# Optimization experiments

Hardware: AMD Instinct MI355X
Metric: run time of the kernel (lower is better)

Reference implementation:

```python
import jax, jax.numpy as jnp
import numpy as np

IN_U = 1024
OUT_U = 1024
BATCH = 4096
HID = 20            # ceil(log2(IN_U*OUT_U)), layer_encoding_dim=0 since num_layers=1
MLP_H = 10
FEAT = 3 + 3 * HID  # 63


def setup_inputs() -> dict:
    key = jax.random.key(0)
    ks = jax.random.split(key, 6)
    X = jax.random.normal(ks[0], (BATCH, IN_U), dtype=jnp.float32)
    weight = jax.random.normal(ks[1], (IN_U, OUT_U), dtype=jnp.float32) * 0.02
    # binary positional encodings per cell (encode_weight_hidden_states)
    k = jnp.arange(IN_U * OUT_U, dtype=jnp.int32).reshape(IN_U, OUT_U)
    shifts = jnp.arange(HID - 1, -1, -1, dtype=jnp.int32)
    hidden = ((k[..., None] >> shifts) & 1).astype(jnp.float32)  # [IN_U, OUT_U, HID]
    W1 = jax.random.normal(ks[2], (FEAT, MLP_H), dtype=jnp.float32) / np.float32(np.sqrt(FEAT))
    b1 = jnp.zeros((MLP_H,), jnp.float32)
    W2 = jax.random.normal(ks[3], (MLP_H, MLP_H), dtype=jnp.float32) / np.float32(np.sqrt(MLP_H))
    b2 = jnp.zeros((MLP_H,), jnp.float32)
    W3 = jax.random.normal(ks[4], (MLP_H, 1 + HID), dtype=jnp.float32) / np.float32(np.sqrt(MLP_H))
    b3 = jnp.zeros((1 + HID,), jnp.float32)
    return {"X": X, "weight": weight, "hidden": hidden,
            "W1": W1, "b1": b1, "W2": W2, "b2": b2, "W3": W3, "b3": b3}


def reference(X, weight, hidden, W1, b1, W2, b2, W3, b3):
    n, m = weight.shape
    # exclude-self column means ('forward') and row means ('backward')
    fwd_mean = (jnp.sum(weight, axis=0, keepdims=True) - weight) / (n - 1)   # [n,m]
    bwd_mean = (jnp.sum(weight, axis=1, keepdims=True) - weight) / (m - 1)   # [n,m]
    fwd_hs = (jnp.sum(hidden, axis=0, keepdims=True) - hidden) / (n - 1)     # [n,m,H]
    bwd_hs = (jnp.sum(hidden, axis=1, keepdims=True) - hidden) / (m - 1)     # [n,m,H]
    feat = jnp.concatenate(
        [weight[..., None], fwd_mean[..., None], bwd_mean[..., None],
         hidden, fwd_hs, bwd_hs], axis=-1)                                   # [n,m,3+3H]
    h = jax.nn.relu(jnp.einsum('nmf,fh->nmh', feat, W1) + b1)
    h = jax.nn.relu(jnp.einsum('nmh,hk->nmk', h, W2) + b2)
    updates = jnp.einsum('nmk,ko->nmo', h, W3) + b3                          # [n,m,1+H]
    new_weight = weight + updates[..., 0]
    # (hidden states also get updates[...,1:] in the torch module, but only the
    #  softmax output is returned)
    logits = jax.nn.relu(X @ new_weight)                                     # [B,m]
    return jax.nn.softmax(logits, axis=-1)
```

## Files before the change

kernel.cpp:

```cpp
#include <hip/hip_runtime.h>
#include <hip/hip_bf16.h>
#include <stdint.h>


#define RS_OFF      0
#define CSPART_OFF  4096
#define BT_OFF      266240
#define AH_OFF      4460544

typedef __attribute__((ext_vector_type(8))) _Float16 f16x8;
typedef __attribute__((ext_vector_type(4))) float f32x4;

__device__ __forceinline__ unsigned short f2h(float x) {
    _Float16 h = (_Float16)x;
    unsigned short u;
    __builtin_memcpy(&u, &h, 2);
    return u;
}
__device__ __forceinline__ float h2f(unsigned short u) {
    _Float16 h;
    __builtin_memcpy(&h, &u, 2);
    return (float)h;
}
__device__ __forceinline__ void gld16(const void* g, void* l) {
    __builtin_amdgcn_global_load_lds(
        (const __attribute__((address_space(1))) unsigned*)g,
        (__attribute__((address_space(3))) unsigned*)l, 16, 0, 0);
}

__global__ __launch_bounds__(256) void k_pre(const float* __restrict__ w,
        float* __restrict__ rs, float* __restrict__ cs_part) {
    __shared__ float part[4][1024];
    int t = threadIdx.x;
    int lane = t & 63, wv = t >> 6;
    int r0 = blockIdx.x * 16 + wv * 4;
    float ccol[16];
    #pragma unroll
    for (int j = 0; j < 16; ++j) ccol[j] = 0.f;
    #pragma unroll
    for (int rr = 0; rr < 4; ++rr) {
        int row = r0 + rr;
        float rsum = 0.f;
        #pragma unroll
        for (int j = 0; j < 16; ++j) {
            float v = w[(size_t)row * 1024 + j * 64 + lane];
            ccol[j] += v;
            rsum += v;
        }
        #pragma unroll
        for (int o = 32; o; o >>= 1) rsum += __shfl_down(rsum, o);
        if (lane == 0) rs[row] = rsum;
    }
    #pragma unroll
    for (int j = 0; j < 16; ++j) part[wv][j * 64 + lane] = ccol[j];
    __syncthreads();
    #pragma unroll
    for (int j = 0; j < 4; ++j) {
        int c = t + j * 256;
        cs_part[(size_t)blockIdx.x * 1024 + c] =
            part[0][c] + part[1][c] + part[2][c] + part[3][c];
    }
}

__global__ __launch_bounds__(256) void k_nw(const float* __restrict__ w,
        const float* __restrict__ X,
        const float* __restrict__ rs, const float* __restrict__ cs_part,
        const float* __restrict__ W1, const float* __restrict__ b1,
        const float* __restrict__ W2, const float* __restrict__ b2,
        const float* __restrict__ W3, const float* __restrict__ b3,
        unsigned short* __restrict__ Bt, unsigned short* __restrict__ Ah) {
    __shared__ float sW1[630], sW2[100], sb1[10], sb2[10], sw3[10], sa[10];
    __shared__ float rs_loc[32], cs_loc[32];
    __shared__ float rn_loc[320], cm_loc[320];
    __shared__ float st[32][33];
    int t = threadIdx.x;
    if (blockIdx.x >= 1024) {
        int b2x = blockIdx.x - 1024;
        #pragma unroll
        for (int p = 0; p < 4; ++p) {
            size_t idx = (size_t)b2x * 4096 + p * 1024 + t * 4;
            float4 v = *(const float4*)&X[idx];
            ushort4 h;
            h.x = f2h(v.x); h.y = f2h(v.y); h.z = f2h(v.z); h.w = f2h(v.w);
            *(ushort4*)&Ah[idx] = h;
        }
        return;
    }
    int n0 = (blockIdx.x & 31) * 32;
    int m0 = (blockIdx.x >> 5) * 32;
    const float inv = 1.0f / 1023.0f;

    for (int i = t; i < 630; i += 256) sW1[i] = W1[i];
    if (t < 100) sW2[t] = W2[t];
    if (t >= 128 && t < 138) { sb1[t - 128] = b1[t - 128]; sb2[t - 128] = b2[t - 128]; }
    if (t >= 160 && t < 170) sw3[t - 160] = W3[(t - 160) * 21];
    if (t >= 192 && t < 224) rs_loc[t - 192] = rs[n0 + t - 192];
    if (t >= 224 && t < 256) {
        float s = 0.f;
        #pragma unroll
        for (int p = 0; p < 64; ++p) s += cs_part[(size_t)p * 1024 + m0 + (t - 224)];
        cs_loc[t - 224] = s;
    }
    float b30 = b3[0];
    __syncthreads();
    if (t < 10) sa[t] = sW1[t] - (sW1[10 + t] + sW1[20 + t]) * inv;
    for (int id = t; id < 640; id += 256) {
        int h = id % 10, i = (id / 10) & 31, side = id >= 320;
        if (!side) {
            int n = n0 + i;
            float v = rs_loc[i] * sW1[20 + h] * inv;
            #pragma unroll
            for (int j = 0; j < 10; j++) {
                float bit = (float)((n >> (9 - j)) & 1);
                v += bit * (sW1[(3 + j) * 10 + h] + sW1[(43 + j) * 10 + h]
                            - sW1[(23 + j) * 10 + h] * inv);
                v += (512.0f * inv) * sW1[(23 + j) * 10 + h];
            }
            rn_loc[i * 10 + h] = v;
        } else {
            int m = m0 + i;
            float v = cs_loc[i] * sW1[10 + h] * inv + sb1[h];
            #pragma unroll
            for (int j = 0; j < 10; j++) {
                float bit = (float)((m >> (9 - j)) & 1);
                v += bit * (sW1[(13 + j) * 10 + h] + sW1[(33 + j) * 10 + h]
                            - sW1[(53 + j) * 10 + h] * inv);
                v += (512.0f * inv) * sW1[(53 + j) * 10 + h];
            }
            cm_loc[i * 10 + h] = v;
        }
    }
    __syncthreads();
    int ml = t & 31;
    #pragma unroll
    for (int i = 0; i < 4; i++) {
        int nl = (t >> 5) + 8 * i;
        float wv = w[(size_t)(n0 + nl) * 1024 + m0 + ml];
        float h1[10];
        #pragma unroll
        for (int h = 0; h < 10; h++)
            h1[h] = fmaxf(wv * sa[h] + rn_loc[nl * 10 + h] + cm_loc[ml * 10 + h], 0.f);
        float u = b30;
        #pragma unroll
        for (int k = 0; k < 10; k++) {
            float h2 = sb2[k];
            #pragma unroll
            for (int h = 0; h < 10; h++) h2 += h1[h] * sW2[h * 10 + k];
            u += fmaxf(h2, 0.f) * sw3[k];
        }
        st[nl][ml] = wv + u;
    }
    __syncthreads();
    int mrow = t >> 3, kc = t & 7;
    unsigned short hi4[4], lo4[4];
    #pragma unroll
    for (int j = 0; j < 4; j++) {
        float v = st[kc * 4 + j][mrow];
        unsigned short h = f2h(v);
        hi4[j] = h;
        lo4[j] = f2h(v - h2f(h));
    }
    size_t base = (size_t)(m0 + mrow) * 2048 + n0 + kc * 4;
    *(ushort4*)&Bt[base]        = make_ushort4(hi4[0], hi4[1], hi4[2], hi4[3]);
    *(ushort4*)&Bt[base + 1024] = make_ushort4(lo4[0], lo4[1], lo4[2], lo4[3]);
}

__global__ __launch_bounds__(256, 3) void k_gemm6(const unsigned short* __restrict__ Ah,
        const unsigned short* __restrict__ Bt, float* __restrict__ out) {
    __shared__ unsigned short sAh[128 * 64];
    __shared__ unsigned short sBh[64 * 64], sBl[64 * 64];
    int tid = threadIdx.x;
    int lane = tid & 63, w = tid >> 6;
    int b = blockIdx.x;
    int xcd = b & 7, s = b >> 3;
    int ty = (xcd << 2) | (s >> 4);
    int tx = s & 15;
    int n0 = tx * 64, m0 = ty * 128;
    int wm = (w >> 1) * 64, wn = (w & 1) * 32;
    int quad = lane >> 4, l16 = lane & 15;

    f32x4 acc[4][2];
    #pragma unroll
    for (int i = 0; i < 4; i++)
        #pragma unroll
        for (int j = 0; j < 2; j++) acc[i][j] = (f32x4)0.f;

    for (int it = 0; it < 16; ++it) {
        int kb = it * 64;
        __syncthreads();
        #pragma unroll
        for (int s2 = 0; s2 < 4; ++s2) {
            int P = s2 * 256 + tid;
            int row = P >> 3;
            int seg = (P & 7) ^ (row & 7);
            int ldsOff = (s2 * 256 + w * 64) * 8;
            size_t ga = (size_t)(m0 + row) * 1024 + kb + seg * 8;
            gld16(&Ah[ga], &sAh[ldsOff]);
        }
        #pragma unroll
        for (int s2 = 0; s2 < 2; ++s2) {
            int P = s2 * 256 + tid;
            int row = P >> 3;
            int seg = (P & 7) ^ (row & 7);
            int ldsOff = (s2 * 256 + w * 64) * 8;
            size_t gb = (size_t)(n0 + row) * 2048 + kb + seg * 8;
            gld16(&Bt[gb], &sBh[ldsOff]);
            gld16(&Bt[gb + 1024], &sBl[ldsOff]);
        }
        __syncthreads();
        #pragma unroll
        for (int ks = 0; ks < 2; ++ks) {
            int segk = ks * 4 + quad;
            f16x8 ah[4], bh[2], bl[2];
            #pragma unroll
            for (int i = 0; i < 4; ++i) {
                int ra = wm + i * 16 + l16;
                int ca = (ra * 8 + (segk ^ (ra & 7))) * 8;
                ah[i] = *(const f16x8*)&sAh[ca];
            }
            #pragma unroll
            for (int j = 0; j < 2; ++j) {
                int rb = wn + j * 16 + l16;
                int cb = (rb * 8 + (segk ^ (rb & 7))) * 8;
                bh[j] = *(const f16x8*)&sBh[cb];
                bl[j] = *(const f16x8*)&sBl[cb];
            }
            #pragma unroll
            for (int i = 0; i < 4; ++i)
                #pragma unroll
                for (int j = 0; j < 2; ++j) {
                    acc[i][j] = __builtin_amdgcn_mfma_f32_16x16x32_f16(ah[i], bh[j], acc[i][j], 0, 0, 0);
                    acc[i][j] = __builtin_amdgcn_mfma_f32_16x16x32_f16(ah[i], bl[j], acc[i][j], 0, 0, 0);
                }
        }
    }
    #pragma unroll
    for (int i = 0; i < 4; ++i) {
        int mr = m0 + wm + i * 16 + quad * 4;
        #pragma unroll
        for (int j = 0; j < 2; ++j) {
            int nc = n0 + wn + j * 16 + l16;
            #pragma unroll
            for (int r = 0; r < 4; ++r)
                out[(size_t)(mr + r) * 1024 + nc] = fmaxf(acc[i][j][r], 0.f);
        }
    }
}

__global__ __launch_bounds__(256) void k_softmax2(float* __restrict__ C) {
    int row = blockIdx.x, t = threadIdx.x, lane = t & 63, wv = t >> 6;
    __shared__ float red[8];
    float4 v = *(float4*)&C[(size_t)row * 1024 + t * 4];
    float lm = fmaxf(fmaxf(v.x, v.y), fmaxf(v.z, v.w));
    #pragma unroll
    for (int o = 32; o; o >>= 1) lm = fmaxf(lm, __shfl_down(lm, o));
    if (lane == 0) red[wv] = lm;
    __syncthreads();
    float mx = fmaxf(fmaxf(red[0], red[1]), fmaxf(red[2], red[3]));
    float4 e;
    e.x = __expf(v.x - mx); e.y = __expf(v.y - mx);
    e.z = __expf(v.z - mx); e.w = __expf(v.w - mx);
    float ls = e.x + e.y + e.z + e.w;
    #pragma unroll
    for (int o = 32; o; o >>= 1) ls += __shfl_down(ls, o);
    if (lane == 0) red[4 + wv] = ls;
    __syncthreads();
    float inv = 1.0f / (red[4] + red[5] + red[6] + red[7]);
    e.x *= inv; e.y *= inv; e.z *= inv; e.w *= inv;
    *(float4*)&C[(size_t)row * 1024 + t * 4] = e;
}

extern "C" void kernel_launch(void* const* d_in, const int* in_sizes, int n_in,
                              void* d_out, int out_size, void* d_ws, size_t ws_size,
                              hipStream_t stream) {
    const float* X  = (const float*)d_in[0];
    const float* W  = (const float*)d_in[1];
    const float* W1 = (const float*)d_in[3];
    const float* b1 = (const float*)d_in[4];
    const float* W2 = (const float*)d_in[5];
    const float* b2 = (const float*)d_in[6];
    const float* W3 = (const float*)d_in[7];
    const float* b3 = (const float*)d_in[8];

    char* wsb = (char*)d_ws;
    float* rs            = (float*)(wsb + RS_OFF);
    float* cs_part       = (float*)(wsb + CSPART_OFF);
    unsigned short* Bt   = (unsigned short*)(wsb + BT_OFF);
    unsigned short* Ah   = (unsigned short*)(wsb + AH_OFF);
    float* out = (float*)d_out;

    k_pre<<<64, 256, 0, stream>>>(W, rs, cs_part);
    k_nw<<<2048, 256, 0, stream>>>(W, X, rs, cs_part, W1, b1, W2, b2, W3, b3, Bt, Ah);
    k_gemm6<<<512, 256, 0, stream>>>(Ah, Bt, out);
    k_softmax2<<<4096, 256, 0, stream>>>(out);
}
```

Baseline: 179.8 us.

## Split GEMM K dimension in two and merge partials in softmax kernel

The GEMM now runs 1024 blocks, each covering half of K (512), and writes raw partial sums to two workspace buffers. The softmax kernel adds the two partials, applies the ReLU, and then runs the softmax. The aim is to fill more CUs and raise occupancy, since only 512 blocks were launched before. In exchange it writes and reads an extra 16 MB partial buffer, which adds memory traffic.

```diff
diff --git a/kernel.cpp b/kernel.cpp
--- a/kernel.cpp
+++ b/kernel.cpp
@@ -7,6 +7,8 @@
 #define CSPART_OFF  4096
 #define BT_OFF      266240
 #define AH_OFF      4460544
+#define C0_OFF      12849152
+#define C1_OFF      29626368
 
 typedef __attribute__((ext_vector_type(8))) _Float16 f16x8;
 typedef __attribute__((ext_vector_type(4))) float f32x4;
@@ -165,17 +167,22 @@
     *(ushort4*)&Bt[base + 1024] = make_ushort4(lo4[0], lo4[1], lo4[2], lo4[3]);
 }
 
-__global__ __launch_bounds__(256, 3) void k_gemm6(const unsigned short* __restrict__ Ah,
-        const unsigned short* __restrict__ Bt, float* __restrict__ out) {
+__global__ __launch_bounds__(256, 4) void k_gemm7(const unsigned short* __restrict__ Ah,
+        const unsigned short* __restrict__ Bt,
+        float* __restrict__ C0, float* __restrict__ C1) {
     __shared__ unsigned short sAh[128 * 64];
     __shared__ unsigned short sBh[64 * 64], sBl[64 * 64];
     int tid = threadIdx.x;
     int lane = tid & 63, w = tid >> 6;
     int b = blockIdx.x;
     int xcd = b & 7, s = b >> 3;
-    int ty = (xcd << 2) | (s >> 4);
-    int tx = s & 15;
+    int half = s >> 6;
+    int s2 = s & 63;
+    int ty = (xcd << 2) | (s2 >> 4);
+    int tx = s2 & 15;
     int n0 = tx * 64, m0 = ty * 128;
+    int k0 = half * 512;
+    float* __restrict__ C = half ? C1 : C0;
     int wm = (w >> 1) * 64, wn = (w & 1) * 32;
     int quad = lane >> 4, l16 = lane & 15;
 
@@ -185,24 +192,24 @@
         #pragma unroll
         for (int j = 0; j < 2; j++) acc[i][j] = (f32x4)0.f;
 
-    for (int it = 0; it < 16; ++it) {
-        int kb = it * 64;
+    for (int it = 0; it < 8; ++it) {
+        int kb = k0 + it * 64;
         __syncthreads();
         #pragma unroll
-        for (int s2 = 0; s2 < 4; ++s2) {
-            int P = s2 * 256 + tid;
+        for (int s3 = 0; s3 < 4; ++s3) {
+            int P = s3 * 256 + tid;
             int row = P >> 3;
             int seg = (P & 7) ^ (row & 7);
-            int ldsOff = (s2 * 256 + w * 64) * 8;
+            int ldsOff = (s3 * 256 + w * 64) * 8;
             size_t ga = (size_t)(m0 + row) * 1024 + kb + seg * 8;
             gld16(&Ah[ga], &sAh[ldsOff]);
         }
         #pragma unroll
-        for (int s2 = 0; s2 < 2; ++s2) {
-            int P = s2 * 256 + tid;
+        for (int s3 = 0; s3 < 2; ++s3) {
+            int P = s3 * 256 + tid;
             int row = P >> 3;
             int seg = (P & 7) ^ (row & 7);
-            int ldsOff = (s2 * 256 + w * 64) * 8;
+            int ldsOff = (s3 * 256 + w * 64) * 8;
             size_t gb = (size_t)(n0 + row) * 2048 + kb + seg * 8;
             gld16(&Bt[gb], &sBh[ldsOff]);
             gld16(&Bt[gb + 1024], &sBl[ldsOff]);
@@ -242,15 +249,23 @@
             int nc = n0 + wn + j * 16 + l16;
             #pragma unroll
             for (int r = 0; r < 4; ++r)
-                out[(size_t)(mr + r) * 1024 + nc] = fmaxf(acc[i][j][r], 0.f);
-        }
-    }
-}
-
-__global__ __launch_bounds__(256) void k_softmax2(float* __restrict__ C) {
+                C[(size_t)(mr + r) * 1024 + nc] = acc[i][j][r];
+        }
+    }
+}
+
+__global__ __launch_bounds__(256) void k_softmax3(const float* __restrict__ C0,
+        const float* __restrict__ C1, float* __restrict__ out) {
     int row = blockIdx.x, t = threadIdx.x, lane = t & 63, wv = t >> 6;
     __shared__ float red[8];
-    float4 v = *(float4*)&C[(size_t)row * 1024 + t * 4];
+    size_t base = (size_t)row * 1024 + t * 4;
+    float4 a = *(const float4*)&C0[base];
+    float4 bq = *(const float4*)&C1[base];
+    float4 v;
+    v.x = fmaxf(a.x + bq.x, 0.f);
+    v.y = fmaxf(a.y + bq.y, 0.f);
+    v.z = fmaxf(a.z + bq.z, 0.f);
+    v.w = fmaxf(a.w + bq.w, 0.f);
     float lm = fmaxf(fmaxf(v.x, v.y), fmaxf(v.z, v.w));
     #pragma unroll
     for (int o = 32; o; o >>= 1) lm = fmaxf(lm, __shfl_down(lm, o));
@@ -267,7 +282,7 @@
     __syncthreads();
     float inv = 1.0f / (red[4] + red[5] + red[6] + red[7]);
     e.x *= inv; e.y *= inv; e.z *= inv; e.w *= inv;
-    *(float4*)&C[(size_t)row * 1024 + t * 4] = e;
+    *(float4*)&out[base] = e;
 }
 
 extern "C" void kernel_launch(void* const* d_in, const int* in_sizes, int n_in,
@@ -287,10 +302,12 @@
     float* cs_part       = (float*)(wsb + CSPART_OFF);
     unsigned short* Bt   = (unsigned short*)(wsb + BT_OFF);
     unsigned short* Ah   = (unsigned short*)(wsb + AH_OFF);
+    float* C0            = (float*)(wsb + C0_OFF);
+    float* C1            = (float*)(wsb + C1_OFF);
     float* out = (float*)d_out;
 
     k_pre<<<64, 256, 0, stream>>>(W, rs, cs_part);
     k_nw<<<2048, 256, 0, stream>>>(W, X, rs, cs_part, W1, b1, W2, b2, W3, b3, Bt, Ah);
-    k_gemm6<<<512, 256, 0, stream>>>(Ah, Bt, out);
-    k_softmax2<<<4096, 256, 0, stream>>>(out);
-}
+    k_gemm7<<<1024, 256, 0, stream>>>(Ah, Bt, C0, C1);
+    k_softmax3<<<4096, 256, 0, stream>>>(C0, C1, out);
+}
```

Result: slower. 184.0 us (+2.3%).
